# Kernel tuning notes

Hardware: AMD Instinct MI355X
Metric: run time of the kernel (lower is better)

Reference implementation:

```python
import jax, jax.numpy as jnp
import numpy as np

D_MODEL = 1024
NUM_HEADS = 16
D_K = D_MODEL // NUM_HEADS


def setup_inputs() -> dict:
    key = jax.random.key(0)
    ks = jax.random.split(key, 11)
    B, S, D = 2, 2048, D_MODEL
    s = 1.0 / np.sqrt(D)  # torch Linear default init scale
    inp = {
        'query': jax.random.normal(ks[0], (B, S, D), jnp.float32),
        'key': jax.random.normal(ks[1], (B, S, D), jnp.float32),
        'value': jax.random.normal(ks[2], (B, S, D), jnp.float32),
        'Wq': jax.random.uniform(ks[3], (D, D), jnp.float32, -s, s),
        'bq': jax.random.uniform(ks[4], (D,), jnp.float32, -s, s),
        'Wk': jax.random.uniform(ks[5], (D, D), jnp.float32, -s, s),
        'bk': jax.random.uniform(ks[6], (D,), jnp.float32, -s, s),
        'Wv': jax.random.uniform(ks[7], (D, D), jnp.float32, -s, s),
        'bv': jax.random.uniform(ks[8], (D,), jnp.float32, -s, s),
        'Wo': jax.random.uniform(ks[9], (D, D), jnp.float32, -s, s),
        'bo': jax.random.uniform(ks[10], (D,), jnp.float32, -s, s),
    }
    return inp


def reference(query, key, value, Wq, bq, Wk, bk, Wv, bv, Wo, bo):
    B, S, D = query.shape
    H, dk = NUM_HEADS, D_K
    # Linear projections (torch Linear: x @ W.T + b), split into heads -> [B,H,S,dk]
    Q = (query @ Wq.T + bq).reshape(B, S, H, dk).transpose(0, 2, 1, 3)
    K = (key @ Wk.T + bk).reshape(B, S, H, dk).transpose(0, 2, 1, 3)
    V = (value @ Wv.T + bv).reshape(B, S, H, dk).transpose(0, 2, 1, 3)
    scale = jnp.sqrt(jnp.asarray(dk, query.dtype))
    scores = jnp.einsum('bhqd,bhkd->bhqk', Q, K) / scale  # [B,H,S,S]
    attn = jax.nn.softmax(scores, axis=-1)
    ctx = jnp.einsum('bhqk,bhkd->bhqd', attn, V)  # [B,H,S,dk]
    ctx = ctx.transpose(0, 2, 1, 3).reshape(B, S, D)
    return ctx @ Wo.T + bo
```

## Files before the change

kernel.cpp:

```cpp
#include <hip/hip_runtime.h>

#define SEQ 2048
#define DM  1024
#define NH  16
#define DK  64
#define BATCH 2
#define MROWS (BATCH * SEQ)
#define PPITCH 72

typedef __attribute__((ext_vector_type(8))) short bf16x8;
typedef __attribute__((ext_vector_type(4))) float f32x4;

extern "C" __device__ float __ocml_native_exp2_f32(float);

__device__ __forceinline__ float bf2f(unsigned short u) {
    union { unsigned int i; float f; } v;
    v.i = ((unsigned int)u) << 16;
    return v.f;
}

__device__ __forceinline__ unsigned short f2bf(float f) {
    union { float f; unsigned int i; } v;
    v.f = f;
    unsigned int r = v.i + 0x7FFFu + ((v.i >> 16) & 1u);
    return (unsigned short)(r >> 16);
}

__device__ __forceinline__ unsigned int pk_trunc(float a, float b) {
    return __builtin_amdgcn_perm(__float_as_uint(b), __float_as_uint(a),
                                 0x07060302u);
}

__device__ __forceinline__ uint4 pack8(float4 x, float4 y) {
    uint4 r;
    r.x = (unsigned)f2bf(x.x) | ((unsigned)f2bf(x.y) << 16);
    r.y = (unsigned)f2bf(x.z) | ((unsigned)f2bf(x.w) << 16);
    r.z = (unsigned)f2bf(y.x) | ((unsigned)f2bf(y.y) << 16);
    r.w = (unsigned)f2bf(y.z) | ((unsigned)f2bf(y.w) << 16);
    return r;
}

__device__ __forceinline__ void gll16(const void* g, void* l) {
    __builtin_amdgcn_global_load_lds(
        (const __attribute__((address_space(1))) unsigned int*)g,
        (__attribute__((address_space(3))) unsigned int*)l, 16, 0, 0);
}

__global__ void detect_dtype(const unsigned short* __restrict__ q,
                             unsigned int* __restrict__ flag) {
    const int lane = threadIdx.x;
    unsigned short u = q[lane * 2];
    int e = (u >> 7) & 0xFF;
    int hit = (e >= 100 && e <= 135) ? 1 : 0;
    unsigned long long m = __ballot(hit);
    if (lane == 0) *flag = (__popcll(m) >= 48) ? 0u : 1u;
}

#define QSCALE 0.1803368801111204f
#define CVT_TOTAL 16781312u
struct CvtArgs {
    const void* src[11];
    unsigned short* dst[11];
};

__global__ __launch_bounds__(256) void convert_all(CvtArgs a,
                                                   const unsigned int* __restrict__ flagp) {
    const unsigned int f = *flagp;
    const size_t e0 = ((size_t)blockIdx.x * 256 + threadIdx.x) * 8;
    if (e0 >= CVT_TOTAL) return;
    const unsigned int cum[12] = {0u, 4194304u, 8388608u, 12582912u, 13631488u,
                                  14680064u, 15728640u, 16777216u, 16778240u,
                                  16779264u, 16780288u, 16781312u};
    int r = 0;
    #pragma unroll
    for (int i = 1; i < 11; ++i) r += (e0 >= cum[i]) ? 1 : 0;
    const size_t local = e0 - cum[r];
    const float sc = (r == 3 || r == 7) ? QSCALE : 1.0f;
    if (f) {
        const float* s = (const float*)a.src[r] + local;
        float4 x = *(const float4*)s;
        float4 y = *(const float4*)(s + 4);
        x.x *= sc; x.y *= sc; x.z *= sc; x.w *= sc;
        y.x *= sc; y.y *= sc; y.z *= sc; y.w *= sc;
        *(uint4*)(a.dst[r] + local) = pack8(x, y);
    } else {
        const unsigned short* s = (const unsigned short*)a.src[r] + local;
        if (sc != 1.0f) {
            unsigned short o[8];
            #pragma unroll
            for (int i = 0; i < 8; ++i) o[i] = f2bf(bf2f(s[i]) * sc);
            *(uint4*)(a.dst[r] + local) = *(const uint4*)o;
        } else {
            *(uint4*)(a.dst[r] + local) = *(const uint4*)s;
        }
    }
}

__device__ __forceinline__ void gemm_core(
    const unsigned short* __restrict__ A, const unsigned short* __restrict__ W,
    const unsigned short* __restrict__ bias, void* __restrict__ C, int cMode)
{
    __shared__ unsigned short Al[128 * 64];
    __shared__ unsigned short Bl[128 * 64];

    const int tid  = threadIdx.x;
    const int w    = tid >> 6;
    const int lane = tid & 63;
    const int lo   = lane & 15;
    const int quad = lane >> 4;
    const int wr   = w >> 1;
    const int wc   = w & 1;
    const int bm   = blockIdx.y * 128;
    const int bn   = blockIdx.x * 128;

    const int r8  = lane >> 3;
    const int csw = ((lane ^ r8) & 7) * 8;
    const unsigned short* gA = A + (size_t)(bm + w * 32 + r8) * DM + csw;
    const unsigned short* gB = W + (size_t)(bn + w * 32 + r8) * DM + csw;
    unsigned short* lA = &Al[(w * 32) * 64];
    unsigned short* lB = &Bl[(w * 32) * 64];

    f32x4 acc[4][4];
    #pragma unroll
    for (int i = 0; i < 4; ++i)
        #pragma unroll
        for (int n = 0; n < 4; ++n) acc[i][n] = (f32x4){0.f, 0.f, 0.f, 0.f};

    const int swz = (lo & 7);

    for (int k0 = 0; k0 < DM; k0 += 64) {
        __syncthreads();
        #pragma unroll
        for (int j = 0; j < 4; ++j) {
            gll16(gA + (size_t)j * 8 * DM + k0, lA + j * 8 * 64);
            gll16(gB + (size_t)j * 8 * DM + k0, lB + j * 8 * 64);
        }
        __syncthreads();

        #pragma unroll
        for (int kc = 0; kc < 2; ++kc) {
            bf16x8 af[4], bfr[4];
            #pragma unroll
            for (int i = 0; i < 4; ++i)
                af[i] = *(const bf16x8*)&Al[(wr * 64 + i * 16 + lo) * 64 +
                                            (((kc * 4 + quad) ^ swz) * 8)];
            #pragma unroll
            for (int n = 0; n < 4; ++n)
                bfr[n] = *(const bf16x8*)&Bl[(wc * 64 + n * 16 + lo) * 64 +
                                             (((kc * 4 + quad) ^ swz) * 8)];
            #pragma unroll
            for (int i = 0; i < 4; ++i)
                #pragma unroll
                for (int n = 0; n < 4; ++n)
                    acc[i][n] = __builtin_amdgcn_mfma_f32_16x16x32_bf16(af[i], bfr[n], acc[i][n], 0, 0, 0);
        }
    }

    float bj[4];
    #pragma unroll
    for (int n = 0; n < 4; ++n)
        bj[n] = bf2f(bias[bn + wc * 64 + n * 16 + lo]);

    if (cMode == 2) {
        #pragma unroll
        for (int i = 0; i < 4; ++i)
            #pragma unroll
            for (int n = 0; n < 4; ++n) {
                const int row0 = bm + wr * 64 + i * 16 + quad * 4;
                const int col  = bn + wc * 64 + n * 16 + lo;
                ushort4 cv;
                cv.x = f2bf(acc[i][n][0] + bj[n]);
                cv.y = f2bf(acc[i][n][1] + bj[n]);
                cv.z = f2bf(acc[i][n][2] + bj[n]);
                cv.w = f2bf(acc[i][n][3] + bj[n]);
                const size_t off = ((size_t)((row0 >> 11) * 16 + (col >> 6)) * 64
                                    + (col & 63)) * 2048 + (row0 & 2047);
                *(ushort4*)((unsigned short*)C + off) = cv;
            }
    } else {
        #pragma unroll
        for (int i = 0; i < 4; ++i)
            #pragma unroll
            for (int n = 0; n < 4; ++n)
                #pragma unroll
                for (int r = 0; r < 4; ++r) {
                    const int row = bm + wr * 64 + i * 16 + quad * 4 + r;
                    const size_t off = (size_t)row * DM + bn + wc * 64 + n * 16 + lo;
                    const float vv = acc[i][n][r] + bj[n];
                    if (cMode == 1) ((float*)C)[off] = vv;
                    else            ((unsigned short*)C)[off] = f2bf(vv);
                }
    }
}

__global__ __launch_bounds__(256, 2) void gemm_qkv(
    const unsigned short* __restrict__ qa, const unsigned short* __restrict__ ka,
    const unsigned short* __restrict__ va,
    const unsigned short* __restrict__ wq, const unsigned short* __restrict__ wk,
    const unsigned short* __restrict__ wv,
    const unsigned short* __restrict__ bq, const unsigned short* __restrict__ bk,
    const unsigned short* __restrict__ bv,
    unsigned short* __restrict__ oq, unsigned short* __restrict__ ok,
    unsigned short* __restrict__ ovT)
{
    if (blockIdx.z == 0)      gemm_core(qa, wq, bq, oq, 0);
    else if (blockIdx.z == 1) gemm_core(ka, wk, bk, ok, 0);
    else                      gemm_core(va, wv, bv, ovT, 2);
}

__global__ __launch_bounds__(256, 2) void gemm_out(
    const unsigned short* __restrict__ A, const unsigned short* __restrict__ W,
    const unsigned short* __restrict__ B, void* __restrict__ C,
    const unsigned int* __restrict__ flagp)
{
    gemm_core(A, W, B, C, (int)*flagp);
}

__global__ __launch_bounds__(256) void attn_mfma6(
    const unsigned short* __restrict__ Q,
    const unsigned short* __restrict__ K,
    const unsigned short* __restrict__ VT,
    unsigned short* __restrict__ CTX)
{
    __shared__ unsigned short Kl[3][64 * 64];
    __shared__ unsigned short Vl[3][64 * 64];
    __shared__ unsigned short Pl[4][2][16 * PPITCH];

    const int tid  = threadIdx.x;
    const int w    = tid >> 6;
    const int lane = tid & 63;
    const int lo   = lane & 15;
    const int quad = lane >> 4;
    const int bh = blockIdx.y;
    const int b  = bh >> 4;
    const int h  = bh & 15;
    const int q0 = blockIdx.x * 128 + w * 32;

    bf16x8 aq[2][2];
    #pragma unroll
    for (int f = 0; f < 2; ++f)
        #pragma unroll
        for (int c = 0; c < 2; ++c)
            aq[f][c] = *(const bf16x8*)(Q + (size_t)(b * SEQ + q0 + f * 16 + lo) * DM
                                        + h * 64 + c * 32 + quad * 8);

    f32x4 o[2][4];
    #pragma unroll
    for (int f = 0; f < 2; ++f)
        #pragma unroll
        for (int dt = 0; dt < 4; ++dt) o[f][dt] = (f32x4){0.f, 0.f, 0.f, 0.f};
    f32x4 lacc[2];
    lacc[0] = (f32x4){0.f, 0.f, 0.f, 0.f};
    lacc[1] = (f32x4){0.f, 0.f, 0.f, 0.f};

    const short one_s = (short)0x3F80;
    const bf16x8 ones = {one_s, one_s, one_s, one_s, one_s, one_s, one_s, one_s};

    const int r8  = lane >> 3;
    const int csw = ((lane ^ r8) & 7) * 8;
    const int swz = lo & 7;
    const unsigned short* Kg = K + (size_t)b * SEQ * DM + h * 64;
    const unsigned short* Vg = VT + (size_t)bh * 64 * 2048;

    #define STAGE(jt, bb) do {                                              \
        const int _jn = (jt) * 64;                                          \
        _Pragma("unroll")                                                   \
        for (int _j = 0; _j < 2; ++_j) {                                    \
            gll16(Kg + (size_t)(_jn + w * 16 + _j * 8 + r8) * DM + csw,     \
                  &Kl[bb][(w * 16 + _j * 8) * 64]);                         \
            gll16(Vg + (size_t)(w * 16 + _j * 8 + r8) * 2048 + _jn + csw,   \
                  &Vl[bb][(w * 16 + _j * 8) * 64]);                         \
        }                                                                   \
    } while (0)

    STAGE(0, 0);
    STAGE(1, 1);
    asm volatile("s_waitcnt vmcnt(4)" ::: "memory");
    __builtin_amdgcn_s_barrier();
    __builtin_amdgcn_sched_barrier(0);

    const int NT = SEQ / 64;
    int cur = 0;
    for (int t = 0; t < NT; ++t) {
        if (t + 2 < NT) {
            const int nb = (cur + 2 >= 3) ? cur - 1 : cur + 2;
            STAGE(t + 2, nb);
        }

        const unsigned short* Kc = Kl[cur];
        const unsigned short* Vc = Vl[cur];

        f32x4 st[4][2];
        __builtin_amdgcn_s_setprio(1);
        #pragma unroll
        for (int kt = 0; kt < 4; ++kt) {
            bf16x8 ak0 = *(const bf16x8*)&Kc[(kt * 16 + lo) * 64 + ((quad ^ swz) * 8)];
            bf16x8 ak1 = *(const bf16x8*)&Kc[(kt * 16 + lo) * 64 + (((4 + quad) ^ swz) * 8)];
            #pragma unroll
            for (int f = 0; f < 2; ++f) {
                f32x4 c = (f32x4){0.f, 0.f, 0.f, 0.f};
                c = __builtin_amdgcn_mfma_f32_16x16x32_bf16(ak0, aq[f][0], c, 0, 0, 0);
                c = __builtin_amdgcn_mfma_f32_16x16x32_bf16(ak1, aq[f][1], c, 0, 0, 0);
                st[kt][f] = c;
            }
        }
        __builtin_amdgcn_s_setprio(0);

        #pragma unroll
        for (int f = 0; f < 2; ++f)
            #pragma unroll
            for (int kt = 0; kt < 4; ++kt) {
                float p0 = __ocml_native_exp2_f32(st[kt][f][0]);
                float p1 = __ocml_native_exp2_f32(st[kt][f][1]);
                float p2 = __ocml_native_exp2_f32(st[kt][f][2]);
                float p3 = __ocml_native_exp2_f32(st[kt][f][3]);
                uint2 pv;
                pv.x = pk_trunc(p0, p1);
                pv.y = pk_trunc(p2, p3);
                *(uint2*)&Pl[w][f][lo * PPITCH + kt * 16 + quad * 4] = pv;
            }
        bf16x8 ap[2][2];
        #pragma unroll
        for (int f = 0; f < 2; ++f)
            #pragma unroll
            for (int c = 0; c < 2; ++c)
                ap[f][c] = *(const bf16x8*)&Pl[w][f][lo * PPITCH + c * 32 + quad * 8];

        __builtin_amdgcn_s_setprio(1);
        #pragma unroll
        for (int f = 0; f < 2; ++f) {
            lacc[f] = __builtin_amdgcn_mfma_f32_16x16x32_bf16(ap[f][0], ones, lacc[f], 0, 0, 0);
            lacc[f] = __builtin_amdgcn_mfma_f32_16x16x32_bf16(ap[f][1], ones, lacc[f], 0, 0, 0);
        }

        #pragma unroll
        for (int dt = 0; dt < 4; ++dt) {
            bf16x8 bv0 = *(const bf16x8*)&Vc[(dt * 16 + lo) * 64 + ((quad ^ swz) * 8)];
            bf16x8 bv1 = *(const bf16x8*)&Vc[(dt * 16 + lo) * 64 + (((4 + quad) ^ swz) * 8)];
            #pragma unroll
            for (int f = 0; f < 2; ++f) {
                o[f][dt] = __builtin_amdgcn_mfma_f32_16x16x32_bf16(ap[f][0], bv0, o[f][dt], 0, 0, 0);
                o[f][dt] = __builtin_amdgcn_mfma_f32_16x16x32_bf16(ap[f][1], bv1, o[f][dt], 0, 0, 0);
            }
        }
        __builtin_amdgcn_s_setprio(0);

        if (t + 2 < NT) {
            asm volatile("s_waitcnt vmcnt(4)" ::: "memory");
        } else {
            asm volatile("s_waitcnt vmcnt(0)" ::: "memory");
        }
        __builtin_amdgcn_s_barrier();
        __builtin_amdgcn_sched_barrier(0);

        cur = (cur == 2) ? 0 : cur + 1;
    }
    #undef STAGE

    #pragma unroll
    for (int f = 0; f < 2; ++f)
        #pragma unroll
        for (int r = 0; r < 4; ++r) {
            const float inv = 1.0f / lacc[f][r];
            const size_t base = (size_t)(b * SEQ + q0 + f * 16 + quad * 4 + r) * DM
                                + h * 64 + lo;
            #pragma unroll
            for (int dt = 0; dt < 4; ++dt)
                CTX[base + dt * 16] = f2bf(o[f][dt][r] * inv);
        }
}

extern "C" void kernel_launch(void* const* d_in, const int* in_sizes, int n_in,
                              void* d_out, int out_size, void* d_ws, size_t ws_size,
                              hipStream_t stream) {
    const size_t E4 = 4194304, E1 = 1048576;
    unsigned short* qb  = (unsigned short*)d_ws;
    unsigned short* kb  = qb  + E4;
    unsigned short* vb  = kb  + E4;
    unsigned short* wqb = vb  + E4;
    unsigned short* wkb = wqb + E1;
    unsigned short* wvb = wkb + E1;
    unsigned short* wob = wvb + E1;
    unsigned short* bqb = wob + E1;
    unsigned short* bkb = bqb + 1024;
    unsigned short* bvb = bkb + 1024;
    unsigned short* bob = bvb + 1024;
    unsigned short* wsQ = bob + 1024;
    unsigned short* wsK = wsQ + E4;
    unsigned short* wsVt = wsK + E4;
    unsigned int*  flag = (unsigned int*)(wsVt + E4);
    unsigned short* wsC = qb;

    detect_dtype<<<1, 64, 0, stream>>>((const unsigned short*)d_in[0], flag);

    CvtArgs ca;
    ca.src[0] = d_in[0];  ca.dst[0] = qb;
    ca.src[1] = d_in[1];  ca.dst[1] = kb;
    ca.src[2] = d_in[2];  ca.dst[2] = vb;
    ca.src[3] = d_in[3];  ca.dst[3] = wqb;
    ca.src[4] = d_in[5];  ca.dst[4] = wkb;
    ca.src[5] = d_in[7];  ca.dst[5] = wvb;
    ca.src[6] = d_in[9];  ca.dst[6] = wob;
    ca.src[7] = d_in[4];  ca.dst[7] = bqb;
    ca.src[8] = d_in[6];  ca.dst[8] = bkb;
    ca.src[9] = d_in[8];  ca.dst[9] = bvb;
    ca.src[10] = d_in[10]; ca.dst[10] = bob;
    convert_all<<<(CVT_TOTAL / 8 + 255) / 256, 256, 0, stream>>>(ca, flag);

    dim3 gq(DM / 128, MROWS / 128, 3);
    gemm_qkv<<<gq, 256, 0, stream>>>(qb, kb, vb, wqb, wkb, wvb,
                                     bqb, bkb, bvb, wsQ, wsK, wsVt);

    dim3 ga(SEQ / 128, BATCH * NH);
    attn_mfma6<<<ga, 256, 0, stream>>>(wsQ, wsK, wsVt, wsC);

    dim3 go(DM / 128, MROWS / 128);
    gemm_out<<<go, 256, 0, stream>>>(wsC, wob, bob, d_out, flag);
}
```

Baseline: 223.6 us.

## Double-buffer GEMM LDS tiles and fold dtype detection into convert kernel

The shared GEMM core now keeps two LDS buffers for A and B and issues the global-to-LDS loads for the next K tile before running the MFMAs on the current one. This replaces the old pattern of two barriers per iteration with a fully exposed load, so memory latency can overlap with compute. Separately, the one-wave dtype detection kernel is removed: every convert block recomputes the flag itself and block 0 writes it for later kernels, saving one launch. The cost is double the LDS per block, which may lower occupancy, plus redundant flag work in each convert block.

```diff
diff --git a/kernel.cpp b/kernel.cpp
--- a/kernel.cpp
+++ b/kernel.cpp
@@ -46,16 +46,6 @@
         (__attribute__((address_space(3))) unsigned int*)l, 16, 0, 0);
 }
 
-__global__ void detect_dtype(const unsigned short* __restrict__ q,
-                             unsigned int* __restrict__ flag) {
-    const int lane = threadIdx.x;
-    unsigned short u = q[lane * 2];
-    int e = (u >> 7) & 0xFF;
-    int hit = (e >= 100 && e <= 135) ? 1 : 0;
-    unsigned long long m = __ballot(hit);
-    if (lane == 0) *flag = (__popcll(m) >= 48) ? 0u : 1u;
-}
-
 #define QSCALE 0.1803368801111204f
 #define CVT_TOTAL 16781312u
 struct CvtArgs {
@@ -64,8 +54,23 @@
 };
 
 __global__ __launch_bounds__(256) void convert_all(CvtArgs a,
-                                                   const unsigned int* __restrict__ flagp) {
-    const unsigned int f = *flagp;
+                                                   const unsigned short* __restrict__ qsrc,
+                                                   unsigned int* __restrict__ flagout) {
+    __shared__ unsigned int sflag;
+    if (threadIdx.x < 64) {
+        unsigned short u = qsrc[threadIdx.x * 2];
+        int e = (u >> 7) & 0xFF;
+        int hit = (e >= 100 && e <= 135) ? 1 : 0;
+        unsigned long long m = __ballot(hit);
+        if (threadIdx.x == 0) {
+            unsigned int fl = (__popcll(m) >= 48) ? 0u : 1u;
+            sflag = fl;
+            if (blockIdx.x == 0) *flagout = fl;
+        }
+    }
+    __syncthreads();
+    const unsigned int f = sflag;
+
     const size_t e0 = ((size_t)blockIdx.x * 256 + threadIdx.x) * 8;
     if (e0 >= CVT_TOTAL) return;
     const unsigned int cum[12] = {0u, 4194304u, 8388608u, 12582912u, 13631488u,
@@ -100,8 +105,8 @@
     const unsigned short* __restrict__ A, const unsigned short* __restrict__ W,
     const unsigned short* __restrict__ bias, void* __restrict__ C, int cMode)
 {
-    __shared__ unsigned short Al[128 * 64];
-    __shared__ unsigned short Bl[128 * 64];
+    __shared__ unsigned short Al[2][128 * 64];
+    __shared__ unsigned short Bl[2][128 * 64];
 
     const int tid  = threadIdx.x;
     const int w    = tid >> 6;
@@ -117,8 +122,16 @@
     const int csw = ((lane ^ r8) & 7) * 8;
     const unsigned short* gA = A + (size_t)(bm + w * 32 + r8) * DM + csw;
     const unsigned short* gB = W + (size_t)(bn + w * 32 + r8) * DM + csw;
-    unsigned short* lA = &Al[(w * 32) * 64];
-    unsigned short* lB = &Bl[(w * 32) * 64];
+
+    #define GSTAGE(k0, bb) do {                                               \
+        _Pragma("unroll")                                                     \
+        for (int _j = 0; _j < 4; ++_j) {                                      \
+            gll16(gA + (size_t)_j * 8 * DM + (k0),                            \
+                  &Al[bb][(w * 32 + _j * 8) * 64]);                           \
+            gll16(gB + (size_t)_j * 8 * DM + (k0),                            \
+                  &Bl[bb][(w * 32 + _j * 8) * 64]);                           \
+        }                                                                     \
+    } while (0)
 
     f32x4 acc[4][4];
     #pragma unroll
@@ -128,33 +141,42 @@
 
     const int swz = (lo & 7);
 
-    for (int k0 = 0; k0 < DM; k0 += 64) {
-        __syncthreads();
-        #pragma unroll
-        for (int j = 0; j < 4; ++j) {
-            gll16(gA + (size_t)j * 8 * DM + k0, lA + j * 8 * 64);
-            gll16(gB + (size_t)j * 8 * DM + k0, lB + j * 8 * 64);
-        }
-        __syncthreads();
+    GSTAGE(0, 0);
+    asm volatile("s_waitcnt vmcnt(0)" ::: "memory");
+    __builtin_amdgcn_s_barrier();
+    __builtin_amdgcn_sched_barrier(0);
+
+    const int NK = DM / 64;
+    #pragma unroll 2
+    for (int t = 0; t < NK; ++t) {
+        const int cur = t & 1;
+        if (t + 1 < NK) GSTAGE((t + 1) * 64, cur ^ 1);
 
         #pragma unroll
         for (int kc = 0; kc < 2; ++kc) {
             bf16x8 af[4], bfr[4];
             #pragma unroll
             for (int i = 0; i < 4; ++i)
-                af[i] = *(const bf16x8*)&Al[(wr * 64 + i * 16 + lo) * 64 +
-                                            (((kc * 4 + quad) ^ swz) * 8)];
+                af[i] = *(const bf16x8*)&Al[cur][(wr * 64 + i * 16 + lo) * 64 +
+                                                 (((kc * 4 + quad) ^ swz) * 8)];
             #pragma unroll
             for (int n = 0; n < 4; ++n)
-                bfr[n] = *(const bf16x8*)&Bl[(wc * 64 + n * 16 + lo) * 64 +
-                                             (((kc * 4 + quad) ^ swz) * 8)];
+                bfr[n] = *(const bf16x8*)&Bl[cur][(wc * 64 + n * 16 + lo) * 64 +
+                                                  (((kc * 4 + quad) ^ swz) * 8)];
             #pragma unroll
             for (int i = 0; i < 4; ++i)
                 #pragma unroll
                 for (int n = 0; n < 4; ++n)
                     acc[i][n] = __builtin_amdgcn_mfma_f32_16x16x32_bf16(af[i], bfr[n], acc[i][n], 0, 0, 0);
         }
+
+        if (t + 1 < NK) {
+            asm volatile("s_waitcnt vmcnt(0)" ::: "memory");
+            __builtin_amdgcn_s_barrier();
+            __builtin_amdgcn_sched_barrier(0);
+        }
     }
+    #undef GSTAGE
 
     float bj[4];
     #pragma unroll
@@ -391,8 +413,6 @@
     unsigned int*  flag = (unsigned int*)(wsVt + E4);
     unsigned short* wsC = qb;
 
-    detect_dtype<<<1, 64, 0, stream>>>((const unsigned short*)d_in[0], flag);
-
     CvtArgs ca;
     ca.src[0] = d_in[0];  ca.dst[0] = qb;
     ca.src[1] = d_in[1];  ca.dst[1] = kb;
@@ -405,7 +425,8 @@
     ca.src[8] = d_in[6];  ca.dst[8] = bkb;
     ca.src[9] = d_in[8];  ca.dst[9] = bvb;
     ca.src[10] = d_in[10]; ca.dst[10] = bob;
-    convert_all<<<(CVT_TOTAL / 8 + 255) / 256, 256, 0, stream>>>(ca, flag);
+    convert_all<<<(CVT_TOTAL / 8 + 255) / 256, 256, 0, stream>>>(
+        ca, (const unsigned short*)d_in[0], flag);
 
     dim3 gq(DM / 128, MROWS / 128, 3);
     gemm_qkv<<<gq, 256, 0, stream>>>(qb, kb, vb, wqb, wkb, wvb,
```

Result: slower. 239.7 us (+7.2%).

## Software-pipeline QK^T of next tile with softmax/PV and fold dtype detection

Applied to the files above, without the earlier changes.

The attention loop now computes QK^T scores for tile t+1 while doing exp, P write and the PV MFMAs for tile t. It uses ping-pong score registers, a 4-deep K buffer and a 3-deep V buffer with separate K and V staging. The goal is to hide MFMA and LDS latency between the two GEMM phases, at the cost of more registers and LDS. The fixed vmcnt(4) wait near the loop tail may not cover the last K loads. Separately, the dtype-detection kernel is merged into the conversion kernel, which saves one launch.

```diff
diff --git a/kernel.cpp b/kernel.cpp
--- a/kernel.cpp
+++ b/kernel.cpp
@@ -46,16 +46,6 @@
         (__attribute__((address_space(3))) unsigned int*)l, 16, 0, 0);
 }
 
-__global__ void detect_dtype(const unsigned short* __restrict__ q,
-                             unsigned int* __restrict__ flag) {
-    const int lane = threadIdx.x;
-    unsigned short u = q[lane * 2];
-    int e = (u >> 7) & 0xFF;
-    int hit = (e >= 100 && e <= 135) ? 1 : 0;
-    unsigned long long m = __ballot(hit);
-    if (lane == 0) *flag = (__popcll(m) >= 48) ? 0u : 1u;
-}
-
 #define QSCALE 0.1803368801111204f
 #define CVT_TOTAL 16781312u
 struct CvtArgs {
@@ -64,8 +54,23 @@
 };
 
 __global__ __launch_bounds__(256) void convert_all(CvtArgs a,
-                                                   const unsigned int* __restrict__ flagp) {
-    const unsigned int f = *flagp;
+                                                   const unsigned short* __restrict__ qsrc,
+                                                   unsigned int* __restrict__ flagout) {
+    __shared__ unsigned int sflag;
+    if (threadIdx.x < 64) {
+        unsigned short u = qsrc[threadIdx.x * 2];
+        int e = (u >> 7) & 0xFF;
+        int hit = (e >= 100 && e <= 135) ? 1 : 0;
+        unsigned long long m = __ballot(hit);
+        if (threadIdx.x == 0) {
+            unsigned int fl = (__popcll(m) >= 48) ? 0u : 1u;
+            sflag = fl;
+            if (blockIdx.x == 0) *flagout = fl;
+        }
+    }
+    __syncthreads();
+    const unsigned int f = sflag;
+
     const size_t e0 = ((size_t)blockIdx.x * 256 + threadIdx.x) * 8;
     if (e0 >= CVT_TOTAL) return;
     const unsigned int cum[12] = {0u, 4194304u, 8388608u, 12582912u, 13631488u,
@@ -216,13 +221,13 @@
     gemm_core(A, W, B, C, (int)*flagp);
 }
 
-__global__ __launch_bounds__(256) void attn_mfma6(
+__global__ __launch_bounds__(256) void attn_mfma7(
     const unsigned short* __restrict__ Q,
     const unsigned short* __restrict__ K,
     const unsigned short* __restrict__ VT,
     unsigned short* __restrict__ CTX)
 {
-    __shared__ unsigned short Kl[3][64 * 64];
+    __shared__ unsigned short Kl[4][64 * 64];
     __shared__ unsigned short Vl[3][64 * 64];
     __shared__ unsigned short Pl[4][2][16 * PPITCH];
 
@@ -262,100 +267,104 @@
     const unsigned short* Kg = K + (size_t)b * SEQ * DM + h * 64;
     const unsigned short* Vg = VT + (size_t)bh * 64 * 2048;
 
-    #define STAGE(jt, bb) do {                                              \
+    #define KSTAGE(jt, bb) do {                                             \
         const int _jn = (jt) * 64;                                          \
         _Pragma("unroll")                                                   \
-        for (int _j = 0; _j < 2; ++_j) {                                    \
+        for (int _j = 0; _j < 2; ++_j)                                      \
             gll16(Kg + (size_t)(_jn + w * 16 + _j * 8 + r8) * DM + csw,     \
                   &Kl[bb][(w * 16 + _j * 8) * 64]);                         \
+    } while (0)
+    #define VSTAGE(jt, bb) do {                                             \
+        const int _jn = (jt) * 64;                                          \
+        _Pragma("unroll")                                                   \
+        for (int _j = 0; _j < 2; ++_j)                                      \
             gll16(Vg + (size_t)(w * 16 + _j * 8 + r8) * 2048 + _jn + csw,   \
                   &Vl[bb][(w * 16 + _j * 8) * 64]);                         \
+    } while (0)
+
+    #define QKCOMP(Kc, ST) do {                                             \
+        __builtin_amdgcn_s_setprio(1);                                      \
+        _Pragma("unroll")                                                   \
+        for (int _kt = 0; _kt < 4; ++_kt) {                                 \
+            bf16x8 _ak0 = *(const bf16x8*)&(Kc)[(_kt * 16 + lo) * 64 + ((quad ^ swz) * 8)]; \
+            bf16x8 _ak1 = *(const bf16x8*)&(Kc)[(_kt * 16 + lo) * 64 + (((4 + quad) ^ swz) * 8)]; \
+            _Pragma("unroll")                                               \
+            for (int _f = 0; _f < 2; ++_f) {                                \
+                f32x4 _c = (f32x4){0.f, 0.f, 0.f, 0.f};                     \
+                _c = __builtin_amdgcn_mfma_f32_16x16x32_bf16(_ak0, aq[_f][0], _c, 0, 0, 0); \
+                _c = __builtin_amdgcn_mfma_f32_16x16x32_bf16(_ak1, aq[_f][1], _c, 0, 0, 0); \
+                (ST)[_kt][_f] = _c;                                         \
+            }                                                               \
         }                                                                   \
+        __builtin_amdgcn_s_setprio(0);                                      \
     } while (0)
 
-    STAGE(0, 0);
-    STAGE(1, 1);
-    asm volatile("s_waitcnt vmcnt(4)" ::: "memory");
+    const int NT = SEQ / 64;
+
+    KSTAGE(0, 0); KSTAGE(1, 1); KSTAGE(2, 2);
+    VSTAGE(0, 0); VSTAGE(1, 1);
+    asm volatile("s_waitcnt vmcnt(2)" ::: "memory");
     __builtin_amdgcn_s_barrier();
-    __builtin_amdgcn_sched_barrier(0);
-
-    const int NT = SEQ / 64;
-    int cur = 0;
-    for (int t = 0; t < NT; ++t) {
-        if (t + 2 < NT) {
-            const int nb = (cur + 2 >= 3) ? cur - 1 : cur + 2;
-            STAGE(t + 2, nb);
-        }
-
-        const unsigned short* Kc = Kl[cur];
-        const unsigned short* Vc = Vl[cur];
-
-        f32x4 st[4][2];
-        __builtin_amdgcn_s_setprio(1);
-        #pragma unroll
-        for (int kt = 0; kt < 4; ++kt) {
-            bf16x8 ak0 = *(const bf16x8*)&Kc[(kt * 16 + lo) * 64 + ((quad ^ swz) * 8)];
-            bf16x8 ak1 = *(const bf16x8*)&Kc[(kt * 16 + lo) * 64 + (((4 + quad) ^ swz) * 8)];
-            #pragma unroll
-            for (int f = 0; f < 2; ++f) {
-                f32x4 c = (f32x4){0.f, 0.f, 0.f, 0.f};
-                c = __builtin_amdgcn_mfma_f32_16x16x32_bf16(ak0, aq[f][0], c, 0, 0, 0);
-                c = __builtin_amdgcn_mfma_f32_16x16x32_bf16(ak1, aq[f][1], c, 0, 0, 0);
-                st[kt][f] = c;
-            }
-        }
-        __builtin_amdgcn_s_setprio(0);
-
-        #pragma unroll
-        for (int f = 0; f < 2; ++f)
-            #pragma unroll
-            for (int kt = 0; kt < 4; ++kt) {
-                float p0 = __ocml_native_exp2_f32(st[kt][f][0]);
-                float p1 = __ocml_native_exp2_f32(st[kt][f][1]);
-                float p2 = __ocml_native_exp2_f32(st[kt][f][2]);
-                float p3 = __ocml_native_exp2_f32(st[kt][f][3]);
-                uint2 pv;
-                pv.x = pk_trunc(p0, p1);
-                pv.y = pk_trunc(p2, p3);
-                *(uint2*)&Pl[w][f][lo * PPITCH + kt * 16 + quad * 4] = pv;
-            }
-        bf16x8 ap[2][2];
-        #pragma unroll
-        for (int f = 0; f < 2; ++f)
-            #pragma unroll
-            for (int c = 0; c < 2; ++c)
-                ap[f][c] = *(const bf16x8*)&Pl[w][f][lo * PPITCH + c * 32 + quad * 8];
-
-        __builtin_amdgcn_s_setprio(1);
-        #pragma unroll
-        for (int f = 0; f < 2; ++f) {
-            lacc[f] = __builtin_amdgcn_mfma_f32_16x16x32_bf16(ap[f][0], ones, lacc[f], 0, 0, 0);
-            lacc[f] = __builtin_amdgcn_mfma_f32_16x16x32_bf16(ap[f][1], ones, lacc[f], 0, 0, 0);
-        }
-
-        #pragma unroll
-        for (int dt = 0; dt < 4; ++dt) {
-            bf16x8 bv0 = *(const bf16x8*)&Vc[(dt * 16 + lo) * 64 + ((quad ^ swz) * 8)];
-            bf16x8 bv1 = *(const bf16x8*)&Vc[(dt * 16 + lo) * 64 + (((4 + quad) ^ swz) * 8)];
-            #pragma unroll
-            for (int f = 0; f < 2; ++f) {
-                o[f][dt] = __builtin_amdgcn_mfma_f32_16x16x32_bf16(ap[f][0], bv0, o[f][dt], 0, 0, 0);
-                o[f][dt] = __builtin_amdgcn_mfma_f32_16x16x32_bf16(ap[f][1], bv1, o[f][dt], 0, 0, 0);
-            }
-        }
-        __builtin_amdgcn_s_setprio(0);
-
-        if (t + 2 < NT) {
-            asm volatile("s_waitcnt vmcnt(4)" ::: "memory");
-        } else {
-            asm volatile("s_waitcnt vmcnt(0)" ::: "memory");
-        }
-        __builtin_amdgcn_s_barrier();
-        __builtin_amdgcn_sched_barrier(0);
-
-        cur = (cur == 2) ? 0 : cur + 1;
+
+    f32x4 stA[4][2], stB[4][2];
+    QKCOMP(Kl[0], stA);
+
+    int vc = 0;
+
+    #define TILEBODY(t_, SP, SN) do {                                       \
+        if ((t_) + 3 < NT) KSTAGE((t_) + 3, ((t_) + 3) & 3);                \
+        if ((t_) + 2 < NT) VSTAGE((t_) + 2, (vc == 0) ? 2 : vc - 1);        \
+        if ((t_) + 1 < NT) QKCOMP(Kl[((t_) + 1) & 3], SN);                  \
+        _Pragma("unroll")                                                   \
+        for (int f = 0; f < 2; ++f)                                         \
+            _Pragma("unroll")                                               \
+            for (int kt = 0; kt < 4; ++kt) {                                \
+                float p0 = __ocml_native_exp2_f32((SP)[kt][f][0]);          \
+                float p1 = __ocml_native_exp2_f32((SP)[kt][f][1]);          \
+                float p2 = __ocml_native_exp2_f32((SP)[kt][f][2]);          \
+                float p3 = __ocml_native_exp2_f32((SP)[kt][f][3]);          \
+                uint2 pv;                                                   \
+                pv.x = pk_trunc(p0, p1);                                    \
+                pv.y = pk_trunc(p2, p3);                                    \
+                *(uint2*)&Pl[w][f][lo * PPITCH + kt * 16 + quad * 4] = pv;  \
+            }                                                               \
+        bf16x8 ap[2][2];                                                    \
+        _Pragma("unroll")                                                   \
+        for (int f = 0; f < 2; ++f)                                         \
+            _Pragma("unroll")                                               \
+            for (int c = 0; c < 2; ++c)                                     \
+                ap[f][c] = *(const bf16x8*)&Pl[w][f][lo * PPITCH + c * 32 + quad * 8]; \
+        __builtin_amdgcn_s_setprio(1);                                      \
+        _Pragma("unroll")                                                   \
+        for (int f = 0; f < 2; ++f) {                                       \
+            lacc[f] = __builtin_amdgcn_mfma_f32_16x16x32_bf16(ap[f][0], ones, lacc[f], 0, 0, 0); \
+            lacc[f] = __builtin_amdgcn_mfma_f32_16x16x32_bf16(ap[f][1], ones, lacc[f], 0, 0, 0); \
+        }                                                                   \
+        const unsigned short* Vc = Vl[vc];                                  \
+        _Pragma("unroll")                                                   \
+        for (int dt = 0; dt < 4; ++dt) {                                    \
+            bf16x8 bv0 = *(const bf16x8*)&Vc[(dt * 16 + lo) * 64 + ((quad ^ swz) * 8)]; \
+            bf16x8 bv1 = *(const bf16x8*)&Vc[(dt * 16 + lo) * 64 + (((4 + quad) ^ swz) * 8)]; \
+            _Pragma("unroll")                                               \
+            for (int f = 0; f < 2; ++f) {                                   \
+                o[f][dt] = __builtin_amdgcn_mfma_f32_16x16x32_bf16(ap[f][0], bv0, o[f][dt], 0, 0, 0); \
+                o[f][dt] = __builtin_amdgcn_mfma_f32_16x16x32_bf16(ap[f][1], bv1, o[f][dt], 0, 0, 0); \
+            }                                                               \
+        }                                                                   \
+        __builtin_amdgcn_s_setprio(0);                                      \
+        asm volatile("s_waitcnt vmcnt(4)" ::: "memory");                    \
+        __builtin_amdgcn_s_barrier();                                       \
+        vc = (vc == 2) ? 0 : vc + 1;                                        \
+    } while (0)
+
+    for (int t = 0; t < NT; t += 2) {
+        TILEBODY(t,     stA, stB);
+        TILEBODY(t + 1, stB, stA);
     }
-    #undef STAGE
+    #undef TILEBODY
+    #undef QKCOMP
+    #undef KSTAGE
+    #undef VSTAGE
 
     #pragma unroll
     for (int f = 0; f < 2; ++f)
@@ -391,8 +400,6 @@
     unsigned int*  flag = (unsigned int*)(wsVt + E4);
     unsigned short* wsC = qb;
 
-    detect_dtype<<<1, 64, 0, stream>>>((const unsigned short*)d_in[0], flag);
-
     CvtArgs ca;
     ca.src[0] = d_in[0];  ca.dst[0] = qb;
     ca.src[1] = d_in[1];  ca.dst[1] = kb;
@@ -405,14 +412,15 @@
     ca.src[8] = d_in[6];  ca.dst[8] = bkb;
     ca.src[9] = d_in[8];  ca.dst[9] = bvb;
     ca.src[10] = d_in[10]; ca.dst[10] = bob;
-    convert_all<<<(CVT_TOTAL / 8 + 255) / 256, 256, 0, stream>>>(ca, flag);
+    convert_all<<<(CVT_TOTAL / 8 + 255) / 256, 256, 0, stream>>>(
+        ca, (const unsigned short*)d_in[0], flag);
 
     dim3 gq(DM / 128, MROWS / 128, 3);
     gemm_qkv<<<gq, 256, 0, stream>>>(qb, kb, vb, wqb, wkb, wvb,
                                      bqb, bkb, bvb, wsQ, wsK, wsVt);
 
     dim3 ga(SEQ / 128, BATCH * NH);
-    attn_mfma6<<<ga, 256, 0, stream>>>(wsQ, wsK, wsVt, wsC);
+    attn_mfma7<<<ga, 256, 0, stream>>>(wsQ, wsK, wsVt, wsC);
 
     dim3 go(DM / 128, MROWS / 128);
     gemm_out<<<go, 256, 0, stream>>>(wsC, wob, bob, d_out, flag);
```

New measurement: 229.5 us. +2.7%, slower.

## Fuse dtype detection into convert kernel and use 8-wave attention blocks

Applied to the files above, without the earlier changes.

The separate single-wave dtype detection launch is removed. Every convert block now recomputes the flag in its first wave and shares it through LDS, and block 0 writes it out for the later GEMM. The attention kernel goes from 4 waves of 32 query rows to 8 waves of 16 query rows per 128-row block, so each wave issues one K/V staging load per tile instead of two. This halves per-wave registers and raises waves per block, aiming at more latency hiding and one fewer launch, at the cost of less K/V fragment reuse per wave and the removal of the sched_barrier hints.

```diff
diff --git a/kernel.cpp b/kernel.cpp
--- a/kernel.cpp
+++ b/kernel.cpp
@@ -46,16 +46,6 @@
         (__attribute__((address_space(3))) unsigned int*)l, 16, 0, 0);
 }
 
-__global__ void detect_dtype(const unsigned short* __restrict__ q,
-                             unsigned int* __restrict__ flag) {
-    const int lane = threadIdx.x;
-    unsigned short u = q[lane * 2];
-    int e = (u >> 7) & 0xFF;
-    int hit = (e >= 100 && e <= 135) ? 1 : 0;
-    unsigned long long m = __ballot(hit);
-    if (lane == 0) *flag = (__popcll(m) >= 48) ? 0u : 1u;
-}
-
 #define QSCALE 0.1803368801111204f
 #define CVT_TOTAL 16781312u
 struct CvtArgs {
@@ -64,8 +54,23 @@
 };
 
 __global__ __launch_bounds__(256) void convert_all(CvtArgs a,
-                                                   const unsigned int* __restrict__ flagp) {
-    const unsigned int f = *flagp;
+                                                   const unsigned short* __restrict__ qsrc,
+                                                   unsigned int* __restrict__ flagout) {
+    __shared__ unsigned int sflag;
+    if (threadIdx.x < 64) {
+        unsigned short u = qsrc[threadIdx.x * 2];
+        int e = (u >> 7) & 0xFF;
+        int hit = (e >= 100 && e <= 135) ? 1 : 0;
+        unsigned long long m = __ballot(hit);
+        if (threadIdx.x == 0) {
+            unsigned int fl = (__popcll(m) >= 48) ? 0u : 1u;
+            sflag = fl;
+            if (blockIdx.x == 0) *flagout = fl;
+        }
+    }
+    __syncthreads();
+    const unsigned int f = sflag;
+
     const size_t e0 = ((size_t)blockIdx.x * 256 + threadIdx.x) * 8;
     if (e0 >= CVT_TOTAL) return;
     const unsigned int cum[12] = {0u, 4194304u, 8388608u, 12582912u, 13631488u,
@@ -216,7 +221,7 @@
     gemm_core(A, W, B, C, (int)*flagp);
 }
 
-__global__ __launch_bounds__(256) void attn_mfma6(
+__global__ __launch_bounds__(512) void attn_mfma8(
     const unsigned short* __restrict__ Q,
     const unsigned short* __restrict__ K,
     const unsigned short* __restrict__ VT,
@@ -224,7 +229,7 @@
 {
     __shared__ unsigned short Kl[3][64 * 64];
     __shared__ unsigned short Vl[3][64 * 64];
-    __shared__ unsigned short Pl[4][2][16 * PPITCH];
+    __shared__ unsigned short Pl[8][16 * PPITCH];
 
     const int tid  = threadIdx.x;
     const int w    = tid >> 6;
@@ -234,24 +239,18 @@
     const int bh = blockIdx.y;
     const int b  = bh >> 4;
     const int h  = bh & 15;
-    const int q0 = blockIdx.x * 128 + w * 32;
-
-    bf16x8 aq[2][2];
-    #pragma unroll
-    for (int f = 0; f < 2; ++f)
-        #pragma unroll
-        for (int c = 0; c < 2; ++c)
-            aq[f][c] = *(const bf16x8*)(Q + (size_t)(b * SEQ + q0 + f * 16 + lo) * DM
-                                        + h * 64 + c * 32 + quad * 8);
-
-    f32x4 o[2][4];
-    #pragma unroll
-    for (int f = 0; f < 2; ++f)
-        #pragma unroll
-        for (int dt = 0; dt < 4; ++dt) o[f][dt] = (f32x4){0.f, 0.f, 0.f, 0.f};
-    f32x4 lacc[2];
-    lacc[0] = (f32x4){0.f, 0.f, 0.f, 0.f};
-    lacc[1] = (f32x4){0.f, 0.f, 0.f, 0.f};
+    const int q0 = blockIdx.x * 128 + w * 16;
+
+    bf16x8 aq[2];
+    #pragma unroll
+    for (int c = 0; c < 2; ++c)
+        aq[c] = *(const bf16x8*)(Q + (size_t)(b * SEQ + q0 + lo) * DM
+                                 + h * 64 + c * 32 + quad * 8);
+
+    f32x4 o[4];
+    #pragma unroll
+    for (int dt = 0; dt < 4; ++dt) o[dt] = (f32x4){0.f, 0.f, 0.f, 0.f};
+    f32x4 lacc = (f32x4){0.f, 0.f, 0.f, 0.f};
 
     const short one_s = (short)0x3F80;
     const bf16x8 ones = {one_s, one_s, one_s, one_s, one_s, one_s, one_s, one_s};
@@ -264,20 +263,16 @@
 
     #define STAGE(jt, bb) do {                                              \
         const int _jn = (jt) * 64;                                          \
-        _Pragma("unroll")                                                   \
-        for (int _j = 0; _j < 2; ++_j) {                                    \
-            gll16(Kg + (size_t)(_jn + w * 16 + _j * 8 + r8) * DM + csw,     \
-                  &Kl[bb][(w * 16 + _j * 8) * 64]);                         \
-            gll16(Vg + (size_t)(w * 16 + _j * 8 + r8) * 2048 + _jn + csw,   \
-                  &Vl[bb][(w * 16 + _j * 8) * 64]);                         \
-        }                                                                   \
+        gll16(Kg + (size_t)(_jn + w * 8 + r8) * DM + csw,                   \
+              &Kl[bb][(w * 8) * 64]);                                       \
+        gll16(Vg + (size_t)(w * 8 + r8) * 2048 + _jn + csw,                 \
+              &Vl[bb][(w * 8) * 64]);                                       \
     } while (0)
 
     STAGE(0, 0);
     STAGE(1, 1);
-    asm volatile("s_waitcnt vmcnt(4)" ::: "memory");
+    asm volatile("s_waitcnt vmcnt(2)" ::: "memory");
     __builtin_amdgcn_s_barrier();
-    __builtin_amdgcn_sched_barrier(0);
 
     const int NT = SEQ / 64;
     int cur = 0;
@@ -290,84 +285,68 @@
         const unsigned short* Kc = Kl[cur];
         const unsigned short* Vc = Vl[cur];
 
-        f32x4 st[4][2];
+        f32x4 st[4];
         __builtin_amdgcn_s_setprio(1);
         #pragma unroll
         for (int kt = 0; kt < 4; ++kt) {
             bf16x8 ak0 = *(const bf16x8*)&Kc[(kt * 16 + lo) * 64 + ((quad ^ swz) * 8)];
             bf16x8 ak1 = *(const bf16x8*)&Kc[(kt * 16 + lo) * 64 + (((4 + quad) ^ swz) * 8)];
-            #pragma unroll
-            for (int f = 0; f < 2; ++f) {
-                f32x4 c = (f32x4){0.f, 0.f, 0.f, 0.f};
-                c = __builtin_amdgcn_mfma_f32_16x16x32_bf16(ak0, aq[f][0], c, 0, 0, 0);
-                c = __builtin_amdgcn_mfma_f32_16x16x32_bf16(ak1, aq[f][1], c, 0, 0, 0);
-                st[kt][f] = c;
-            }
+            f32x4 c = (f32x4){0.f, 0.f, 0.f, 0.f};
+            c = __builtin_amdgcn_mfma_f32_16x16x32_bf16(ak0, aq[0], c, 0, 0, 0);
+            c = __builtin_amdgcn_mfma_f32_16x16x32_bf16(ak1, aq[1], c, 0, 0, 0);
+            st[kt] = c;
         }
         __builtin_amdgcn_s_setprio(0);
 
         #pragma unroll
-        for (int f = 0; f < 2; ++f)
-            #pragma unroll
-            for (int kt = 0; kt < 4; ++kt) {
-                float p0 = __ocml_native_exp2_f32(st[kt][f][0]);
-                float p1 = __ocml_native_exp2_f32(st[kt][f][1]);
-                float p2 = __ocml_native_exp2_f32(st[kt][f][2]);
-                float p3 = __ocml_native_exp2_f32(st[kt][f][3]);
-                uint2 pv;
-                pv.x = pk_trunc(p0, p1);
-                pv.y = pk_trunc(p2, p3);
-                *(uint2*)&Pl[w][f][lo * PPITCH + kt * 16 + quad * 4] = pv;
-            }
-        bf16x8 ap[2][2];
-        #pragma unroll
-        for (int f = 0; f < 2; ++f)
-            #pragma unroll
-            for (int c = 0; c < 2; ++c)
-                ap[f][c] = *(const bf16x8*)&Pl[w][f][lo * PPITCH + c * 32 + quad * 8];
+        for (int kt = 0; kt < 4; ++kt) {
+            float p0 = __ocml_native_exp2_f32(st[kt][0]);
+            float p1 = __ocml_native_exp2_f32(st[kt][1]);
+            float p2 = __ocml_native_exp2_f32(st[kt][2]);
+            float p3 = __ocml_native_exp2_f32(st[kt][3]);
+            uint2 pv;
+            pv.x = pk_trunc(p0, p1);
+            pv.y = pk_trunc(p2, p3);
+            *(uint2*)&Pl[w][lo * PPITCH + kt * 16 + quad * 4] = pv;
+        }
+        bf16x8 ap[2];
+        #pragma unroll
+        for (int c = 0; c < 2; ++c)
+            ap[c] = *(const bf16x8*)&Pl[w][lo * PPITCH + c * 32 + quad * 8];
 
         __builtin_amdgcn_s_setprio(1);
-        #pragma unroll
-        for (int f = 0; f < 2; ++f) {
-            lacc[f] = __builtin_amdgcn_mfma_f32_16x16x32_bf16(ap[f][0], ones, lacc[f], 0, 0, 0);
-            lacc[f] = __builtin_amdgcn_mfma_f32_16x16x32_bf16(ap[f][1], ones, lacc[f], 0, 0, 0);
-        }
+        lacc = __builtin_amdgcn_mfma_f32_16x16x32_bf16(ap[0], ones, lacc, 0, 0, 0);
+        lacc = __builtin_amdgcn_mfma_f32_16x16x32_bf16(ap[1], ones, lacc, 0, 0, 0);
 
         #pragma unroll
         for (int dt = 0; dt < 4; ++dt) {
             bf16x8 bv0 = *(const bf16x8*)&Vc[(dt * 16 + lo) * 64 + ((quad ^ swz) * 8)];
             bf16x8 bv1 = *(const bf16x8*)&Vc[(dt * 16 + lo) * 64 + (((4 + quad) ^ swz) * 8)];
-            #pragma unroll
-            for (int f = 0; f < 2; ++f) {
-                o[f][dt] = __builtin_amdgcn_mfma_f32_16x16x32_bf16(ap[f][0], bv0, o[f][dt], 0, 0, 0);
-                o[f][dt] = __builtin_amdgcn_mfma_f32_16x16x32_bf16(ap[f][1], bv1, o[f][dt], 0, 0, 0);
-            }
+            o[dt] = __builtin_amdgcn_mfma_f32_16x16x32_bf16(ap[0], bv0, o[dt], 0, 0, 0);
+            o[dt] = __builtin_amdgcn_mfma_f32_16x16x32_bf16(ap[1], bv1, o[dt], 0, 0, 0);
         }
         __builtin_amdgcn_s_setprio(0);
 
         if (t + 2 < NT) {
-            asm volatile("s_waitcnt vmcnt(4)" ::: "memory");
+            asm volatile("s_waitcnt vmcnt(2)" ::: "memory");
         } else {
             asm volatile("s_waitcnt vmcnt(0)" ::: "memory");
         }
         __builtin_amdgcn_s_barrier();
-        __builtin_amdgcn_sched_barrier(0);
 
         cur = (cur == 2) ? 0 : cur + 1;
     }
     #undef STAGE
 
     #pragma unroll
-    for (int f = 0; f < 2; ++f)
-        #pragma unroll
-        for (int r = 0; r < 4; ++r) {
-            const float inv = 1.0f / lacc[f][r];
-            const size_t base = (size_t)(b * SEQ + q0 + f * 16 + quad * 4 + r) * DM
-                                + h * 64 + lo;
-            #pragma unroll
-            for (int dt = 0; dt < 4; ++dt)
-                CTX[base + dt * 16] = f2bf(o[f][dt][r] * inv);
-        }
+    for (int r = 0; r < 4; ++r) {
+        const float inv = 1.0f / lacc[r];
+        const size_t base = (size_t)(b * SEQ + q0 + quad * 4 + r) * DM
+                            + h * 64 + lo;
+        #pragma unroll
+        for (int dt = 0; dt < 4; ++dt)
+            CTX[base + dt * 16] = f2bf(o[dt][r] * inv);
+    }
 }
 
 extern "C" void kernel_launch(void* const* d_in, const int* in_sizes, int n_in,
@@ -391,8 +370,6 @@
     unsigned int*  flag = (unsigned int*)(wsVt + E4);
     unsigned short* wsC = qb;
 
-    detect_dtype<<<1, 64, 0, stream>>>((const unsigned short*)d_in[0], flag);
-
     CvtArgs ca;
     ca.src[0] = d_in[0];  ca.dst[0] = qb;
     ca.src[1] = d_in[1];  ca.dst[1] = kb;
@@ -405,14 +382,15 @@
     ca.src[8] = d_in[6];  ca.dst[8] = bkb;
     ca.src[9] = d_in[8];  ca.dst[9] = bvb;
     ca.src[10] = d_in[10]; ca.dst[10] = bob;
-    convert_all<<<(CVT_TOTAL / 8 + 255) / 256, 256, 0, stream>>>(ca, flag);
+    convert_all<<<(CVT_TOTAL / 8 + 255) / 256, 256, 0, stream>>>(
+        ca, (const unsigned short*)d_in[0], flag);
 
     dim3 gq(DM / 128, MROWS / 128, 3);
     gemm_qkv<<<gq, 256, 0, stream>>>(qb, kb, vb, wqb, wkb, wvb,
                                      bqb, bkb, bvb, wsQ, wsK, wsVt);
 
     dim3 ga(SEQ / 128, BATCH * NH);
-    attn_mfma6<<<ga, 256, 0, stream>>>(wsQ, wsK, wsVt, wsC);
+    attn_mfma8<<<ga, 512, 0, stream>>>(wsQ, wsK, wsVt, wsC);
 
     dim3 go(DM / 128, MROWS / 128);
     gemm_out<<<go, 256, 0, stream>>>(wsC, wob, bob, d_out, flag);
```

Measured after the change: 226.4 us, median of 2. Within noise of the previous version (+1.2%).
